# Kernel tuning notes

Measured on AMD Instinct MI355X. Metric: run time of the kernel, lower is better.

Reference implementation:

```python
import jax, jax.numpy as jnp
import numpy as np


def _xcorr3x3_valid(x, k):
    # x: [B,H,W], k: [B,3,3] per-sample kernel; cross-correlation (matches F.conv2d), VALID padding
    B, H, W = x.shape
    out = jnp.zeros((B, H - 2, W - 2), dtype=x.dtype)
    for u in range(3):
        for v in range(3):
            out = out + x[:, u:u + H - 2, v:v + W - 2] * k[:, u, v, None, None]
    return out


def setup_inputs() -> dict:
    key = jax.random.key(0)
    ks = jax.random.split(key, 4)
    B, H, W = 256, 256, 256
    pred = jax.random.normal(ks[0], (B, H, W), dtype=jnp.float32)
    rhs = jax.random.normal(ks[1], (B, H - 2, W - 2), dtype=jnp.float32)
    Laplace_kernel = jax.random.normal(ks[2], (B, 3, 3), dtype=jnp.float32)
    Df_dr_kernel = jax.random.normal(ks[3], (B, 3, 3), dtype=jnp.float32)
    # physically sensible meshgrids: R in [1,2] (avoids div-by-zero), Z in [-1,1]
    r = jnp.linspace(1.0, 2.0, W, dtype=jnp.float32)
    z = jnp.linspace(-1.0, 1.0, H, dtype=jnp.float32)
    RR = jnp.broadcast_to(r[None, None, :], (B, H, W)).astype(jnp.float32)
    ZZ = jnp.broadcast_to(z[None, :, None], (B, H, W)).astype(jnp.float32)
    Gauss_kernel = (jnp.array([[1., 2., 1.], [2., 4., 2.], [1., 2., 1.]], dtype=jnp.float32) / 16.0)
    return {"pred": pred, "rhs": rhs, "Laplace_kernel": Laplace_kernel,
            "Df_dr_kernel": Df_dr_kernel, "RR": RR, "ZZ": ZZ, "Gauss_kernel": Gauss_kernel}


def reference(pred, rhs, Laplace_kernel, Df_dr_kernel, RR, ZZ, Gauss_kernel):
    # Lpsi, Dpsi_dr: per-sample 3x3 VALID stencils -> [B, H-2, W-2]
    Lpsi = _xcorr3x3_valid(pred, Laplace_kernel)
    Dpsi_dr = -_xcorr3x3_valid(pred, Df_dr_kernel)
    Dpsi_dr = Dpsi_dr / RR[:, 1:-1, 1:-1]
    lhs = Lpsi - Dpsi_dr
    hr = (RR[:, 1, 2] - RR[:, 1, 1])[:, None, None]
    hz = (ZZ[:, 2, 1] - ZZ[:, 1, 1])[:, None, None]
    alfa = -2.0 * (hr ** 2 + hz ** 2)
    GS_ope = lhs * alfa / (hr ** 2 * hz ** 2)
    # Gaussian smoothing, shared kernel, SAME padding (cross-correlation; kernel is symmetric)
    sm = jax.lax.conv_general_dilated(
        GS_ope[:, None, :, :], Gauss_kernel[None, None, :, :],
        window_strides=(1, 1), padding='SAME')
    GS_ope_smooth = -sm
    rhs_computed = -GS_ope_smooth[:, 0, :, :]
    return jnp.mean((rhs_computed - rhs) ** 2)
```

## Files before the change

kernel.cpp:

```cpp
#include <hip/hip_runtime.h>


__global__ __launch_bounds__(256, 4)
void pde_loss_kernel(const float* __restrict__ pred,
                     const float* __restrict__ rhs,
                     const float* __restrict__ KL,
                     const float* __restrict__ KD,
                     const float* __restrict__ RR,
                     const float* __restrict__ ZZ,
                     float* __restrict__ out,
                     float inv_n)
{
    constexpr int H = 256, W = 256, OH = 254, OW = 254;
    const int tid = threadIdx.x;
    const int l   = tid & 63;
    const int wv  = tid >> 6;
    const int b   = blockIdx.x >> 2;
    const int strip = (blockIdx.x & 3) * 4 + wv;
    const int o0 = strip * 16;
    const int o1 = (o0 + 16 < OH) ? (o0 + 16) : OH;

    const size_t ib = (size_t)b * H * W;
    const float* predb = pred + ib;
    const float* rhsb  = rhs + (size_t)b * OH * OW;

    const float hr  = RR[ib + W + 2] - RR[ib + W + 1];
    const float hz  = ZZ[ib + 2 * W + 1] - ZZ[ib + W + 1];
    const float hr2 = hr * hr, hz2 = hz * hz;
    const float s   = -2.0f * (hr2 + hz2) / (hr2 * hz2);

    const int c0 = 4 * l;
    float4 c4[9];
    {
        float4 invr;
        invr.x = 1.0f / RR[ib + W + (c0 + 1)];
        invr.y = 1.0f / RR[ib + W + (c0 + 2)];
        invr.z = 1.0f / RR[ib + W + (c0 + 3)];
        invr.w = 1.0f / RR[ib + W + ((c0 + 4 < W) ? (c0 + 4) : (W - 1))];
        const float* kl = KL + b * 9;
        const float* kd = KD + b * 9;
#pragma unroll
        for (int t = 0; t < 9; ++t) {
            const float a = kl[t] * s, d = kd[t] * s;
            c4[t].x = fmaf(d, invr.x, a);
            c4[t].y = fmaf(d, invr.y, a);
            c4[t].z = fmaf(d, invr.z, a);
            c4[t].w = fmaf(d, invr.w, a);
        }
    }

    const int g0 = o0 - 1;
    float4 pa = make_float4(0.f, 0.f, 0.f, 0.f), pb, pc;
    if (g0 >= 0) pa = *(const float4*)(predb + (size_t)g0 * W + c0);
    pb = *(const float4*)(predb + (size_t)(g0 + 1) * W + c0);
    pc = *(const float4*)(predb + (size_t)(g0 + 2) * W + c0);
    float nxa = __shfl(pa.x, l + 1, 64), nya = __shfl(pa.y, l + 1, 64);
    float nxb = __shfl(pb.x, l + 1, 64), nyb = __shfl(pb.y, l + 1, 64);

    float4 ghA = make_float4(0.f, 0.f, 0.f, 0.f);
    float4 ghB = make_float4(0.f, 0.f, 0.f, 0.f);
    float2 rc0 = make_float2(0.f, 0.f), rc1 = make_float2(0.f, 0.f);
    float acc = 0.0f;

    for (int g = g0; g <= o1; ++g) {
        float4 pn = make_float4(0.f, 0.f, 0.f, 0.f);
        const int rowp = g + 3;
        if (rowp < H && rowp <= o1 + 2)
            pn = *(const float4*)(predb + (size_t)rowp * W + c0);

        float2 rn0 = make_float2(0.f, 0.f), rn1 = make_float2(0.f, 0.f);
        if (g >= o0 && g < o1) {
            const float* rrow = rhsb + (size_t)g * OW + c0;
            rn0 = *(const float2*)rrow;
            if (c0 + 2 < OW) rn1 = *(const float2*)(rrow + 2);
        }

        const float nxc = __shfl(pc.x, l + 1, 64);
        const float nyc = __shfl(pc.y, l + 1, 64);

        float4 gs = make_float4(0.f, 0.f, 0.f, 0.f);
        if ((unsigned)g < (unsigned)OH) {
#define ROWC(p, nx, ny, t0)                                              \
            gs.x = fmaf(p.x, c4[t0].x, fmaf(p.y, c4[t0+1].x, fmaf(p.z, c4[t0+2].x, gs.x))); \
            gs.y = fmaf(p.y, c4[t0].y, fmaf(p.z, c4[t0+1].y, fmaf(p.w, c4[t0+2].y, gs.y))); \
            gs.z = fmaf(p.z, c4[t0].z, fmaf(p.w, c4[t0+1].z, fmaf(nx,  c4[t0+2].z, gs.z))); \
            gs.w = fmaf(p.w, c4[t0].w, fmaf(nx,  c4[t0+1].w, fmaf(ny,  c4[t0+2].w, gs.w)));
            ROWC(pa, nxa, nya, 0)
            ROWC(pb, nxb, nyb, 3)
            ROWC(pc, nxc, nyc, 6)
#undef ROWC
            if (l == 63) { gs.z = 0.f; gs.w = 0.f; }
        }

        float up = __shfl(gs.w, l - 1, 64);
        const float dn = __shfl(gs.x, l + 1, 64);
        if (l == 0) up = 0.f;
        float4 gh;
        gh.x = fmaf(2.f, gs.x, up   + gs.y);
        gh.y = fmaf(2.f, gs.y, gs.x + gs.z);
        gh.z = fmaf(2.f, gs.z, gs.y + gs.w);
        gh.w = fmaf(2.f, gs.w, gs.z + dn);

        const int i = g - 1;
        if (i >= o0 && i < o1) {
            const float smx = (ghA.x + 2.f * ghB.x + gh.x) * 0.0625f;
            const float smy = (ghA.y + 2.f * ghB.y + gh.y) * 0.0625f;
            const float smz = (ghA.z + 2.f * ghB.z + gh.z) * 0.0625f;
            const float smw = (ghA.w + 2.f * ghB.w + gh.w) * 0.0625f;
            const float dx = smx - rc0.x;
            const float dy = smy - rc0.y;
            float dz = smz - rc1.x;
            float dw = smw - rc1.y;
            if (c0 + 2 >= OW) { dz = 0.f; dw = 0.f; }
            acc = fmaf(dx, dx, acc);
            acc = fmaf(dy, dy, acc);
            acc = fmaf(dz, dz, acc);
            acc = fmaf(dw, dw, acc);
        }

        pa = pb; pb = pc; pc = pn;
        nxa = nxb; nya = nyb; nxb = nxc; nyb = nyc;
        ghA = ghB; ghB = gh;
        rc0 = rn0; rc1 = rn1;
    }

#pragma unroll
    for (int off = 32; off > 0; off >>= 1)
        acc += __shfl_down(acc, off, 64);
    __shared__ float wsum[4];
    if (l == 0) wsum[wv] = acc;
    __syncthreads();
    if (tid == 0) {
        const float t = (wsum[0] + wsum[1]) + (wsum[2] + wsum[3]);
        atomicAdd(out, t * inv_n);
    }
}

extern "C" void kernel_launch(void* const* d_in, const int* in_sizes, int n_in,
                              void* d_out, int out_size, void* d_ws, size_t ws_size,
                              hipStream_t stream) {
    const float* pred = (const float*)d_in[0];
    const float* rhs  = (const float*)d_in[1];
    const float* KL   = (const float*)d_in[2];
    const float* KD   = (const float*)d_in[3];
    const float* RR   = (const float*)d_in[4];
    const float* ZZ   = (const float*)d_in[5];
    float* out = (float*)d_out;

    const int B = in_sizes[2] / 9;
    const float inv_n = 1.0f / ((float)B * 254.0f * 254.0f);

    hipMemsetAsync(out, 0, sizeof(float), stream);
    pde_loss_kernel<<<dim3(B * 4), dim3(256), 0, stream>>>(pred, rhs, KL, KD, RR, ZZ, out, inv_n);
}
```

Measured before the change: 223.6 us.

## Halve row strips per wave and load halo columns instead of shuffling

Each wave now processes 8 output rows instead of 16, and the grid doubles to 8 blocks per sample. The launch bound is raised to target 8 blocks per CU. This adds parallelism and occupancy, at the cost of more halo rows being reloaded at strip boundaries. Neighbor-column values are now fetched with an extra float2 global load per row instead of two cross-lane shuffles, trading shuffle latency for extra (mostly cache-hit) memory traffic.

```diff
diff --git a/kernel.cpp b/kernel.cpp
--- a/kernel.cpp
+++ b/kernel.cpp
@@ -1,7 +1,7 @@
 #include <hip/hip_runtime.h>
 
 
-__global__ __launch_bounds__(256, 4)
+__global__ __launch_bounds__(256, 8)
 void pde_loss_kernel(const float* __restrict__ pred,
                      const float* __restrict__ rhs,
                      const float* __restrict__ KL,
@@ -15,10 +15,10 @@
     const int tid = threadIdx.x;
     const int l   = tid & 63;
     const int wv  = tid >> 6;
-    const int b   = blockIdx.x >> 2;
-    const int strip = (blockIdx.x & 3) * 4 + wv;
-    const int o0 = strip * 16;
-    const int o1 = (o0 + 16 < OH) ? (o0 + 16) : OH;
+    const int b   = blockIdx.x >> 3;
+    const int strip = (blockIdx.x & 7) * 4 + wv;
+    const int o0 = strip * 8;
+    const int o1 = (o0 + 8 < OH) ? (o0 + 8) : OH;
 
     const size_t ib = (size_t)b * H * W;
     const float* predb = pred + ib;
@@ -30,6 +30,7 @@
     const float s   = -2.0f * (hr2 + hz2) / (hr2 * hz2);
 
     const int c0 = 4 * l;
+    const int hcol = (c0 + 4 < W) ? (c0 + 4) : (W - 2);
     float4 c4[9];
     {
         float4 invr;
@@ -51,11 +52,15 @@
 
     const int g0 = o0 - 1;
     float4 pa = make_float4(0.f, 0.f, 0.f, 0.f), pb, pc;
-    if (g0 >= 0) pa = *(const float4*)(predb + (size_t)g0 * W + c0);
+    float2 ha = make_float2(0.f, 0.f), hb, hc;
+    if (g0 >= 0) {
+        pa = *(const float4*)(predb + (size_t)g0 * W + c0);
+        ha = *(const float2*)(predb + (size_t)g0 * W + hcol);
+    }
     pb = *(const float4*)(predb + (size_t)(g0 + 1) * W + c0);
+    hb = *(const float2*)(predb + (size_t)(g0 + 1) * W + hcol);
     pc = *(const float4*)(predb + (size_t)(g0 + 2) * W + c0);
-    float nxa = __shfl(pa.x, l + 1, 64), nya = __shfl(pa.y, l + 1, 64);
-    float nxb = __shfl(pb.x, l + 1, 64), nyb = __shfl(pb.y, l + 1, 64);
+    hc = *(const float2*)(predb + (size_t)(g0 + 2) * W + hcol);
 
     float4 ghA = make_float4(0.f, 0.f, 0.f, 0.f);
     float4 ghB = make_float4(0.f, 0.f, 0.f, 0.f);
@@ -64,9 +69,12 @@
 
     for (int g = g0; g <= o1; ++g) {
         float4 pn = make_float4(0.f, 0.f, 0.f, 0.f);
+        float2 hn = make_float2(0.f, 0.f);
         const int rowp = g + 3;
-        if (rowp < H && rowp <= o1 + 2)
+        if (rowp < H && rowp <= o1 + 2) {
             pn = *(const float4*)(predb + (size_t)rowp * W + c0);
+            hn = *(const float2*)(predb + (size_t)rowp * W + hcol);
+        }
 
         float2 rn0 = make_float2(0.f, 0.f), rn1 = make_float2(0.f, 0.f);
         if (g >= o0 && g < o1) {
@@ -75,19 +83,16 @@
             if (c0 + 2 < OW) rn1 = *(const float2*)(rrow + 2);
         }
 
-        const float nxc = __shfl(pc.x, l + 1, 64);
-        const float nyc = __shfl(pc.y, l + 1, 64);
-
         float4 gs = make_float4(0.f, 0.f, 0.f, 0.f);
         if ((unsigned)g < (unsigned)OH) {
-#define ROWC(p, nx, ny, t0)                                              \
+#define ROWC(p, h, t0)                                                   \
             gs.x = fmaf(p.x, c4[t0].x, fmaf(p.y, c4[t0+1].x, fmaf(p.z, c4[t0+2].x, gs.x))); \
             gs.y = fmaf(p.y, c4[t0].y, fmaf(p.z, c4[t0+1].y, fmaf(p.w, c4[t0+2].y, gs.y))); \
-            gs.z = fmaf(p.z, c4[t0].z, fmaf(p.w, c4[t0+1].z, fmaf(nx,  c4[t0+2].z, gs.z))); \
-            gs.w = fmaf(p.w, c4[t0].w, fmaf(nx,  c4[t0+1].w, fmaf(ny,  c4[t0+2].w, gs.w)));
-            ROWC(pa, nxa, nya, 0)
-            ROWC(pb, nxb, nyb, 3)
-            ROWC(pc, nxc, nyc, 6)
+            gs.z = fmaf(p.z, c4[t0].z, fmaf(p.w, c4[t0+1].z, fmaf(h.x, c4[t0+2].z, gs.z))); \
+            gs.w = fmaf(p.w, c4[t0].w, fmaf(h.x, c4[t0+1].w, fmaf(h.y, c4[t0+2].w, gs.w)));
+            ROWC(pa, ha, 0)
+            ROWC(pb, hb, 3)
+            ROWC(pc, hc, 6)
 #undef ROWC
             if (l == 63) { gs.z = 0.f; gs.w = 0.f; }
         }
@@ -119,7 +124,7 @@
         }
 
         pa = pb; pb = pc; pc = pn;
-        nxa = nxb; nya = nyb; nxb = nxc; nyb = nyc;
+        ha = hb; hb = hc; hc = hn;
         ghA = ghB; ghB = gh;
         rc0 = rn0; rc1 = rn1;
     }
@@ -151,5 +156,5 @@
     const float inv_n = 1.0f / ((float)B * 254.0f * 254.0f);
 
     hipMemsetAsync(out, 0, sizeof(float), stream);
-    pde_loss_kernel<<<dim3(B * 4), dim3(256), 0, stream>>>(pred, rhs, KL, KD, RR, ZZ, out, inv_n);
+    pde_loss_kernel<<<dim3(B * 8), dim3(256), 0, stream>>>(pred, rhs, KL, KD, RR, ZZ, out, inv_n);
 }
```

Result: slower. 365.5 us (+63.5%).
